# Kernel tuning notes

Measured on AMD Instinct MI355X. Metric: run time of the kernel, lower is better.

Reference implementation:

```python
import jax, jax.numpy as jnp
import numpy as np

T_TOTAL = 90  # t_total init arg (static decode length)


def _gru_cell(x, h, w_ih, w_hh, b_ih, b_hh):
    # PyTorch nn.GRUCell math
    gi = x @ w_ih.T + b_ih
    gh = h @ w_hh.T + b_hh
    i_r, i_z, i_n = jnp.split(gi, 3, axis=-1)
    h_r, h_z, h_n = jnp.split(gh, 3, axis=-1)
    r = jax.nn.sigmoid(i_r + h_r)
    z = jax.nn.sigmoid(i_z + h_z)
    n = jnp.tanh(i_n + r * h_n)
    return (1.0 - z) * n + z * h


def setup_inputs() -> dict:
    key = jax.random.key(0)
    T, B, NX, H, NZ = 90, 2048, 144, 128, 128
    M1, M2 = 300, 200
    ks = jax.random.split(key, 24)
    def p(k, shape):
        return jax.random.normal(k, shape, dtype=jnp.float32) * 0.05
    return {
        "x": jax.random.normal(ks[0], (T, B, NX), dtype=jnp.float32),
        # encoder GRUCell (nx -> H)
        "w_ih_e": p(ks[1], (3 * H, NX)), "w_hh_e": p(ks[2], (3 * H, H)),
        "b_ih_e": p(ks[3], (3 * H,)),   "b_hh_e": p(ks[4], (3 * H,)),
        # encoder MLP (tanh) H->300->200
        "W1e": p(ks[5], (M1, H)),  "b1e": p(ks[6], (M1,)),
        "W2e": p(ks[7], (M2, M1)), "b2e": p(ks[8], (M2,)),
        # latent heads 200->NZ
        "Wmu": p(ks[9], (NZ, M2)),  "bmu": p(ks[10], (NZ,)),
        "Wlv": p(ks[11], (NZ, M2)), "blv": p(ks[12], (NZ,)),
        # decoder GRUCell (nx+nz -> H)
        "w_ih_d": p(ks[13], (3 * H, NX + NZ)), "w_hh_d": p(ks[14], (3 * H, H)),
        "b_ih_d": p(ks[15], (3 * H,)),          "b_hh_d": p(ks[16], (3 * H,)),
        # decoder MLP (tanh) H->300->200 and output 200->nx
        "W1d": p(ks[17], (M1, H)),  "b1d": p(ks[18], (M1,)),
        "W2d": p(ks[19], (M2, M1)), "b2d": p(ks[20], (M2,)),
        "Wo": p(ks[21], (NX, M2)),  "bo": p(ks[22], (NX,)),
    }


def reference(x, w_ih_e, w_hh_e, b_ih_e, b_hh_e, W1e, b1e, W2e, b2e,
              Wmu, bmu, Wlv, blv, w_ih_d, w_hh_d, b_ih_d, b_hh_d,
              W1d, b1d, W2d, b2d, Wo, bo):
    B = x.shape[1]
    H = w_hh_e.shape[1]
    h0 = jnp.zeros((B, H), dtype=x.dtype)

    # ---- encode: GRU over time, take last hidden ----
    def enc_step(h, xt):
        return _gru_cell(xt, h, w_ih_e, w_hh_e, b_ih_e, b_hh_e), None
    h_x, _ = jax.lax.scan(enc_step, h0, x)  # (B, H)
    he = jnp.tanh(h_x @ W1e.T + b1e)
    he = jnp.tanh(he @ W2e.T + b2e)
    mu = he @ Wmu.T + bmu
    logvar = he @ Wlv.T + blv
    z = mu  # eval mode: z = mu (no reparameterization noise)

    def dec_step(carry, _):
        hd, xp = carry
        rnn_in = jnp.concatenate([xp, z], axis=1)  # (B, NX+NZ)
        hd = _gru_cell(rnn_in, hd, w_ih_d, w_hh_d, b_ih_d, b_hh_d)
        m = jnp.tanh(hd @ W1d.T + b1d)
        m = jnp.tanh(m @ W2d.T + b2d)
        xi = m @ Wo.T + bo
        return (hd, xi), xi

    _, x_rec = jax.lax.scan(dec_step, (h0, x[0]), None, length=T_TOTAL)
    return x_rec, mu, logvar
```

## Files before the change

kernel.cpp:

```cpp
#include <hip/hip_runtime.h>
#include <cstddef>

#define T_STEPS 90
#define BT      2048
#define NXV     144
#define HV      128
#define NZV     128
#define M1V     300
#define M2V     200
#define NB      16
#define NTH     512

typedef __attribute__((ext_vector_type(8))) _Float16 half8v;
typedef __attribute__((ext_vector_type(4))) float f32x4;

constexpr int MTa[12]   = {24,24,19,13, 8, 8,24,24,24,19,13, 9};
constexpr int MREAL[12] = {384,384,300,200,128,128,384,384,384,300,200,144};
constexpr int KREAL[12] = {144,128,128,300,200,200,144,128,128,128,300,200};
constexpr int RSW[12]   = {144,128,128,300,200,200,272,272,128,128,300,200};
constexpr int COW[12]   = {  0,  0,  0,  0,  0,  0,  0,144,  0,  0,  0,  0};
constexpr int P13[13]   = {0,120,240,335,465,521,577,697,817,937,1032,1162,1225};
constexpr int NFRAG = 1225;

__device__ __forceinline__ float fsig(float v)  { return 1.0f / (1.0f + __expf(-v)); }
__device__ __forceinline__ float ftanh(float v) { return 1.0f - 2.0f / (__expf(2.0f * v) + 1.0f); }

__global__ void __launch_bounds__(64)
prep_frags(const float* __restrict__ w_ih_e, const float* __restrict__ w_hh_e,
           const float* __restrict__ W1e,    const float* __restrict__ W2e,
           const float* __restrict__ Wmu,    const float* __restrict__ Wlv,
           const float* __restrict__ w_ih_d, const float* __restrict__ w_hh_d,
           const float* __restrict__ W1d,    const float* __restrict__ W2d,
           const float* __restrict__ Wo,
           const float* __restrict__ b_ih_e, const float* __restrict__ b_hh_e,
           const float* __restrict__ b1e,    const float* __restrict__ b2e,
           const float* __restrict__ bmu,    const float* __restrict__ blv,
           const float* __restrict__ b_ih_d, const float* __restrict__ b_hh_d,
           const float* __restrict__ b1d,    const float* __restrict__ b2d,
           const float* __restrict__ bo,
           _Float16* __restrict__ ws)
{
    int f = blockIdx.x;
    int g = 0;
    while (g < 11 && f >= P13[g + 1]) ++g;
    int fl = f - P13[g];
    int MT = MTa[g];
    int kt = fl / MT, mt = fl - kt * MT;

    const float* W; const float* bias;
    switch (g) {
        case 0:  W = w_ih_e; bias = b_ih_e; break;
        case 1:  W = w_hh_e; bias = b_hh_e; break;
        case 2:  W = W1e;    bias = b1e;    break;
        case 3:  W = W2e;    bias = b2e;    break;
        case 4:  W = Wmu;    bias = bmu;    break;
        case 5:  W = Wlv;    bias = blv;    break;
        case 6:  W = w_ih_d; bias = nullptr; break;
        case 7:  W = w_ih_d; bias = b_ih_d; break;
        case 8:  W = w_hh_d; bias = b_hh_d; break;
        case 9:  W = W1d;    bias = b1d;    break;
        case 10: W = W2d;    bias = b2d;    break;
        default: W = Wo;     bias = bo;     break;
    }
    int l = threadIdx.x;
    int m  = mt * 16 + (l & 15);
    int kb = kt * 32 + (l >> 4) * 8;
    _Float16* dst = ws + (size_t)f * 512 + (size_t)l * 8;
    #pragma unroll
    for (int j = 0; j < 8; ++j) {
        int k = kb + j;
        float val = 0.0f;
        if (m < MREAL[g]) {
            if (k < KREAL[g]) val = W[(size_t)m * RSW[g] + COW[g] + k];
            else if (k == KREAL[g] && bias) val = bias[m];
        }
        dst[j] = (_Float16)val;
    }
}

template<int RS>
__device__ __forceinline__ void gate_gemm_reg(const half8v (&gw)[15],
                                              const _Float16* __restrict__ Bt,
                                              int l, f32x4 (&acc)[3])
{
    const int bo_ = (l & 15) * RS + ((l >> 4) << 3);
    #pragma unroll
    for (int kt = 0; kt < 5; ++kt) {
        half8v bf = *(const half8v*)(Bt + bo_ + kt * 32);
        #pragma unroll
        for (int j = 0; j < 3; ++j)
            acc[j] = __builtin_amdgcn_mfma_f32_16x16x32_f16(gw[kt * 3 + j], bf, acc[j], 0, 0, 0);
    }
}

template<int MT, int KT, int NT, int RS>
__device__ __forceinline__ void mlp_stream(const half8v* __restrict__ A,
                                           const _Float16* __restrict__ Bt,
                                           int w, int l, f32x4 (&acc)[NT])
{
    half8v af[NT * KT];
    #pragma unroll
    for (int i = 0; i < NT; ++i) {
        int mt = w + 8 * i;
        if (mt < MT) {
            #pragma unroll
            for (int kt = 0; kt < KT; ++kt)
                af[i * KT + kt] = A[(size_t)(kt * MT + mt) * 64 + l];
        }
    }
    const int bo_ = (l & 15) * RS + ((l >> 4) << 3);
    #pragma unroll
    for (int kt = 0; kt < KT; ++kt) {
        half8v bf = *(const half8v*)(Bt + bo_ + kt * 32);
        #pragma unroll
        for (int i = 0; i < NT; ++i) {
            int mt = w + 8 * i;
            if (mt < MT)
                acc[i] = __builtin_amdgcn_mfma_f32_16x16x32_f16(af[i * KT + kt], bf, acc[i], 0, 0, 0);
        }
    }
}

template<int MT, int KT, int NT, int RS>
__device__ __forceinline__ void mlp_lds(const _Float16* __restrict__ Alds,
                                        const _Float16* __restrict__ Bt,
                                        int w, int l, f32x4 (&acc)[NT])
{
    const int bo_ = (l & 15) * RS + ((l >> 4) << 3);
    #pragma unroll
    for (int kt = 0; kt < KT; ++kt) {
        half8v bf = *(const half8v*)(Bt + bo_ + kt * 32);
        #pragma unroll
        for (int i = 0; i < NT; ++i) {
            int mt = w + 8 * i;
            if (mt < MT) {
                half8v af = *(const half8v*)(Alds + ((size_t)(kt * MT + mt) * 64 + l) * 8);
                acc[i] = __builtin_amdgcn_mfma_f32_16x16x32_f16(af, bf, acc[i], 0, 0, 0);
            }
        }
    }
}

template<int MT, int NT, int RS>
__device__ __forceinline__ void write_tanhN(const f32x4 (&acc)[NT], int Mreal,
                                            _Float16* __restrict__ T, int w, int l)
{
    int b = l & 15, q4 = (l >> 4) << 2;
    #pragma unroll
    for (int i = 0; i < NT; ++i) {
        int mt = w + 8 * i;
        if (mt < MT) {
            #pragma unroll
            for (int r = 0; r < 4; ++r) {
                int m = mt * 16 + q4 + r;
                if (m < Mreal) T[b * RS + m] = (_Float16)ftanh(acc[i][r]);
            }
        }
    }
}

__global__ void __launch_bounds__(NTH, 2)
vae_mfma(const float* __restrict__ x, const half8v* __restrict__ wsv,
         float* __restrict__ out)
{
    __shared__ __align__(16) _Float16 xT [NB * 168];
    __shared__ __align__(16) _Float16 hT [NB * 168];
    __shared__ __align__(16) _Float16 m1T[NB * 328];
    __shared__ __align__(16) _Float16 m2T[NB * 232];
    __shared__ __align__(16) _Float16 g10L[130 * 512];

    const int tid = threadIdx.x;
    const int w = tid >> 6, l = tid & 63;
    const int bbase = blockIdx.x * NB;
    const size_t XREC_SZ = (size_t)T_STEPS * BT * NXV;
    const size_t MU_OFF = XREC_SZ;
    const size_t LV_OFF = XREC_SZ + (size_t)BT * NZV;
    const f32x4 z4 = {0.f, 0.f, 0.f, 0.f};

#define AHI(g) (wsv + (size_t)P13[g] * 64)

    auto load_x = [&](int t, float xr[5]) {
        #pragma unroll
        for (int u = 0; u < 5; ++u) {
            int i = u * NTH + tid;
            if (i < NB * NXV)
                xr[u] = __builtin_nontemporal_load(
                    &x[(size_t)t * (BT * NXV) + (size_t)(bbase + i / NXV) * NXV + (i % NXV)]);
        }
    };
    auto store_x = [&](const float xr[5]) {
        #pragma unroll
        for (int u = 0; u < 5; ++u) {
            int i = u * NTH + tid;
            if (i < NB * NXV) {
                int b2 = i / NXV, k = i - b2 * NXV;
                xT[b2 * 168 + k] = (_Float16)xr[u];
            }
        }
    };

    half8v gih[15], ghh[15];
    auto load_gates = [&](const half8v* Gih, const half8v* Ghh) {
        #pragma unroll
        for (int kt = 0; kt < 5; ++kt) {
            #pragma unroll
            for (int j = 0; j < 3; ++j) {
                gih[kt * 3 + j] = Gih[(size_t)(kt * 24 + w + 8 * j) * 64 + l];
                ghh[kt * 3 + j] = Ghh[(size_t)(kt * 24 + w + 8 * j) * 64 + l];
            }
        }
    };

    float hreg[4] = {0.f, 0.f, 0.f, 0.f};
    auto gru_combine = [&](const f32x4 (&ai)[3], const f32x4 (&ah)[3]) {
        #pragma unroll
        for (int r = 0; r < 4; ++r) {
            float rr = fsig(ai[0][r] + ah[0][r]);
            float zz = fsig(ai[1][r] + ah[1][r]);
            float nn = ftanh(ai[2][r] + rr * ah[2][r]);
            hreg[r] = (1.f - zz) * nn + zz * hreg[r];
        }
    };
    auto write_h = [&]() {
        int jb = 16 * w + ((l >> 4) << 2), b = l & 15;
        #pragma unroll
        for (int r = 0; r < 4; ++r) hT[b * 168 + jb + r] = (_Float16)hreg[r];
    };

    for (int i = tid; i < NB * 168; i += NTH) { xT[i] = (_Float16)0.f; hT[i] = (_Float16)0.f; }
    for (int i = tid; i < NB * 328; i += NTH) m1T[i] = (_Float16)0.f;
    for (int i = tid; i < NB * 232; i += NTH) m2T[i] = (_Float16)0.f;
    for (int i = tid; i < 130 * 64; i += NTH)
        *(half8v*)(g10L + (size_t)i * 8) = AHI(10)[i];
    load_gates(AHI(0), AHI(1));
    float xr[5] = {0, 0, 0, 0, 0};
    load_x(0, xr);
    __syncthreads();
    if (tid < NB) {
        xT [tid * 168 + 144] = (_Float16)1.f;
        hT [tid * 168 + 128] = (_Float16)1.f;
        m1T[tid * 328 + 300] = (_Float16)1.f;
        m2T[tid * 232 + 200] = (_Float16)1.f;
    }
    store_x(xr);
    load_x(1, xr);
    __syncthreads();

    for (int t = 0; t < T_STEPS; ++t) {
        f32x4 ai[3] = {z4, z4, z4}, ah[3] = {z4, z4, z4};
        gate_gemm_reg<168>(gih, xT, l, ai);
        gate_gemm_reg<168>(ghh, hT, l, ah);
        gru_combine(ai, ah);
        __syncthreads();
        write_h();
        if (t + 1 < T_STEPS) {
            store_x(xr);
            if (t + 2 < T_STEPS) load_x(t + 2, xr);
        }
        __syncthreads();
    }

    {
        f32x4 a1[3] = {z4, z4, z4};
        mlp_stream<19, 5, 3, 168>(AHI(2), hT, w, l, a1);
        write_tanhN<19, 3, 328>(a1, M1V, m1T, w, l);
        __syncthreads();
        f32x4 a2[2] = {z4, z4};
        mlp_stream<13, 10, 2, 328>(AHI(3), m1T, w, l, a2);
        write_tanhN<13, 2, 232>(a2, M2V, m2T, w, l);
        __syncthreads();
        f32x4 am[1] = {z4}, av[1] = {z4};
        mlp_stream<8, 7, 1, 232>(AHI(4), m2T, w, l, am);
        mlp_stream<8, 7, 1, 232>(AHI(5), m2T, w, l, av);
        __syncthreads();
        int b = l & 15, q4 = (l >> 4) << 2;
        int m = w * 16 + q4;
        __builtin_nontemporal_store(am[0], (f32x4*)&out[MU_OFF + (size_t)(bbase + b) * NZV + m]);
        __builtin_nontemporal_store(av[0], (f32x4*)&out[LV_OFF + (size_t)(bbase + b) * NZV + m]);
        #pragma unroll
        for (int r = 0; r < 4; ++r)
            m1T[b * 328 + m + r] = (_Float16)am[0][r];
    }

    f32x4 gzr[3] = {z4, z4, z4};
    {
        for (int i = tid; i < NB * HV; i += NTH) {
            int b2 = i >> 7, j = i & 127;
            hT[b2 * 168 + j] = (_Float16)0.f;
        }
        if (tid < NB) m1T[tid * 328 + 128] = (_Float16)1.f;
        float xr0[5] = {0, 0, 0, 0, 0};
        load_x(0, xr0);
        store_x(xr0);
        __syncthreads();
        mlp_stream<24, 5, 3, 328>(AHI(7), m1T, w, l, gzr);
        load_gates(AHI(6), AHI(8));
        #pragma unroll
        for (int r = 0; r < 4; ++r) hreg[r] = 0.f;
    }
    __syncthreads();

    for (int t = 0; t < T_STEPS; ++t) {
        f32x4 ai[3], ah[3];
        #pragma unroll
        for (int i = 0; i < 3; ++i) { ai[i] = gzr[i]; ah[i] = z4; }
        gate_gemm_reg<168>(gih, xT, l, ai);
        gate_gemm_reg<168>(ghh, hT, l, ah);
        gru_combine(ai, ah);
        __syncthreads();
        write_h();
        __syncthreads();
        f32x4 a1[3] = {z4, z4, z4};
        mlp_stream<19, 5, 3, 168>(AHI(9), hT, w, l, a1);
        write_tanhN<19, 3, 328>(a1, M1V, m1T, w, l);
        __syncthreads();
        f32x4 a2[2] = {z4, z4};
        mlp_lds<13, 10, 2, 328>(g10L, m1T, w, l, a2);
        write_tanhN<13, 2, 232>(a2, M2V, m2T, w, l);
        __syncthreads();
        f32x4 ao[2] = {z4, z4};
        mlp_stream<9, 7, 2, 232>(AHI(11), m2T, w, l, ao);
        {
            int b = l & 15, q4 = (l >> 4) << 2;
            #pragma unroll
            for (int i2 = 0; i2 < 2; ++i2) {
                int mt = w + 8 * i2;
                if (mt < 9) {
                    int m = mt * 16 + q4;
                    __builtin_nontemporal_store(ao[i2],
                        (f32x4*)&out[(size_t)t * (BT * NXV) + (size_t)(bbase + b) * NXV + m]);
                    #pragma unroll
                    for (int r = 0; r < 4; ++r)
                        xT[b * 168 + m + r] = (_Float16)ao[i2][r];
                }
            }
        }
        __syncthreads();
    }
#undef AHI
}

extern "C" void kernel_launch(void* const* d_in, const int* in_sizes, int n_in,
                              void* d_out, int out_size, void* d_ws, size_t ws_size,
                              hipStream_t stream) {
    (void)in_sizes; (void)n_in; (void)out_size; (void)ws_size;
    const float* p[23];
    for (int i = 0; i < 23; ++i) p[i] = (const float*)d_in[i];
    _Float16* ws = (_Float16*)d_ws;

    prep_frags<<<dim3(NFRAG), dim3(64), 0, stream>>>(
        p[1], p[2], p[5], p[7], p[9], p[11], p[13], p[14], p[17], p[19], p[21],
        p[3], p[4], p[6], p[8], p[10], p[12], p[15], p[16], p[18], p[20], p[22],
        ws);

    vae_mfma<<<dim3(BT / NB), dim3(NTH), 0, stream>>>(
        p[0], (const half8v*)ws, (float*)d_out);
}
```

Before: 882.5 us.

## Double-buffer GRU hidden/input LDS tiles to drop a barrier per step

Adds ping-pong buffers for the hidden and input tiles in LDS, so each GRU step writes the new state into the other buffer and one __syncthreads per timestep can be removed in both encoder and decoder loops. It also vectorises the x loads (float4) and the fp16 LDS stores (half4), and shrinks the LDS-resident W2d fragment cache by one K-tile, streaming the last tile from global memory before the MFMA to cut LDS footprint. The cost is extra LDS for the second buffers and more care about buffer parity at the encoder/decoder handoff.

```diff
diff --git a/kernel.cpp b/kernel.cpp
--- a/kernel.cpp
+++ b/kernel.cpp
@@ -12,6 +12,7 @@
 #define NTH     512
 
 typedef __attribute__((ext_vector_type(8))) _Float16 half8v;
+typedef __attribute__((ext_vector_type(4))) _Float16 half4v;
 typedef __attribute__((ext_vector_type(4))) float f32x4;
 
 constexpr int MTa[12]   = {24,24,19,13, 8, 8,24,24,24,19,13, 9};
@@ -142,7 +143,7 @@
 }
 
 template<int MT, int NT, int RS>
-__device__ __forceinline__ void write_tanhN(const f32x4 (&acc)[NT], int Mreal,
+__device__ __forceinline__ void write_tanhV(const f32x4 (&acc)[NT], int Mreal,
                                             _Float16* __restrict__ T, int w, int l)
 {
     int b = l & 15, q4 = (l >> 4) << 2;
@@ -150,10 +151,12 @@
     for (int i = 0; i < NT; ++i) {
         int mt = w + 8 * i;
         if (mt < MT) {
-            #pragma unroll
-            for (int r = 0; r < 4; ++r) {
-                int m = mt * 16 + q4 + r;
-                if (m < Mreal) T[b * RS + m] = (_Float16)ftanh(acc[i][r]);
+            int m0 = mt * 16 + q4;
+            if (m0 < Mreal) {
+                half4v v;
+                #pragma unroll
+                for (int r = 0; r < 4; ++r) v[r] = (_Float16)ftanh(acc[i][r]);
+                *(half4v*)&T[b * RS + m0] = v;
             }
         }
     }
@@ -163,11 +166,11 @@
 vae_mfma(const float* __restrict__ x, const half8v* __restrict__ wsv,
          float* __restrict__ out)
 {
-    __shared__ __align__(16) _Float16 xT [NB * 168];
-    __shared__ __align__(16) _Float16 hT [NB * 168];
+    __shared__ __align__(16) _Float16 xT [2][NB * 168];
+    __shared__ __align__(16) _Float16 hT [2][NB * 168];
     __shared__ __align__(16) _Float16 m1T[NB * 328];
     __shared__ __align__(16) _Float16 m2T[NB * 232];
-    __shared__ __align__(16) _Float16 g10L[130 * 512];
+    __shared__ __align__(16) _Float16 g10L[117 * 512];
 
     const int tid = threadIdx.x;
     const int w = tid >> 6, l = tid & 63;
@@ -179,22 +182,27 @@
 
 #define AHI(g) (wsv + (size_t)P13[g] * 64)
 
-    auto load_x = [&](int t, float xr[5]) {
-        #pragma unroll
-        for (int u = 0; u < 5; ++u) {
-            int i = u * NTH + tid;
-            if (i < NB * NXV)
-                xr[u] = __builtin_nontemporal_load(
-                    &x[(size_t)t * (BT * NXV) + (size_t)(bbase + i / NXV) * NXV + (i % NXV)]);
-        }
-    };
-    auto store_x = [&](const float xr[5]) {
-        #pragma unroll
-        for (int u = 0; u < 5; ++u) {
-            int i = u * NTH + tid;
-            if (i < NB * NXV) {
-                int b2 = i / NXV, k = i - b2 * NXV;
-                xT[b2 * 168 + k] = (_Float16)xr[u];
+    auto load_x4 = [&](int t, f32x4 xr4[2]) {
+        #pragma unroll
+        for (int uu = 0; uu < 2; ++uu) {
+            int idx = uu * NTH + tid;
+            if (idx < NB * (NXV / 4)) {
+                int b2 = idx / (NXV / 4), k4 = idx - b2 * (NXV / 4);
+                xr4[uu] = __builtin_nontemporal_load(
+                    (const f32x4*)&x[(size_t)t * (BT * NXV) + (size_t)(bbase + b2) * NXV + 4 * k4]);
+            }
+        }
+    };
+    auto store_x4 = [&](_Float16* dst, const f32x4 xr4[2]) {
+        #pragma unroll
+        for (int uu = 0; uu < 2; ++uu) {
+            int idx = uu * NTH + tid;
+            if (idx < NB * (NXV / 4)) {
+                int b2 = idx / (NXV / 4), k4 = idx - b2 * (NXV / 4);
+                half4v v;
+                #pragma unroll
+                for (int r = 0; r < 4; ++r) v[r] = (_Float16)xr4[uu][r];
+                *(half4v*)&dst[b2 * 168 + 4 * k4] = v;
             }
         }
     };
@@ -221,53 +229,57 @@
             hreg[r] = (1.f - zz) * nn + zz * hreg[r];
         }
     };
-    auto write_h = [&]() {
+    auto write_h = [&](int p) {
         int jb = 16 * w + ((l >> 4) << 2), b = l & 15;
-        #pragma unroll
-        for (int r = 0; r < 4; ++r) hT[b * 168 + jb + r] = (_Float16)hreg[r];
-    };
-
-    for (int i = tid; i < NB * 168; i += NTH) { xT[i] = (_Float16)0.f; hT[i] = (_Float16)0.f; }
+        half4v v;
+        #pragma unroll
+        for (int r = 0; r < 4; ++r) v[r] = (_Float16)hreg[r];
+        *(half4v*)&hT[p][b * 168 + jb] = v;
+    };
+
+    for (int i = tid; i < 2 * NB * 168; i += NTH) { ((_Float16*)xT)[i] = (_Float16)0.f; ((_Float16*)hT)[i] = (_Float16)0.f; }
     for (int i = tid; i < NB * 328; i += NTH) m1T[i] = (_Float16)0.f;
     for (int i = tid; i < NB * 232; i += NTH) m2T[i] = (_Float16)0.f;
-    for (int i = tid; i < 130 * 64; i += NTH)
+    for (int i = tid; i < 117 * 64; i += NTH)
         *(half8v*)(g10L + (size_t)i * 8) = AHI(10)[i];
     load_gates(AHI(0), AHI(1));
-    float xr[5] = {0, 0, 0, 0, 0};
-    load_x(0, xr);
+    f32x4 xr4[2] = {z4, z4};
+    load_x4(0, xr4);
     __syncthreads();
     if (tid < NB) {
-        xT [tid * 168 + 144] = (_Float16)1.f;
-        hT [tid * 168 + 128] = (_Float16)1.f;
+        xT[0][tid * 168 + 144] = (_Float16)1.f;
+        xT[1][tid * 168 + 144] = (_Float16)1.f;
+        hT[0][tid * 168 + 128] = (_Float16)1.f;
+        hT[1][tid * 168 + 128] = (_Float16)1.f;
         m1T[tid * 328 + 300] = (_Float16)1.f;
         m2T[tid * 232 + 200] = (_Float16)1.f;
     }
-    store_x(xr);
-    load_x(1, xr);
+    store_x4(xT[0], xr4);
+    load_x4(1, xr4);
     __syncthreads();
 
     for (int t = 0; t < T_STEPS; ++t) {
+        int p = t & 1;
         f32x4 ai[3] = {z4, z4, z4}, ah[3] = {z4, z4, z4};
-        gate_gemm_reg<168>(gih, xT, l, ai);
-        gate_gemm_reg<168>(ghh, hT, l, ah);
+        gate_gemm_reg<168>(gih, xT[p], l, ai);
+        gate_gemm_reg<168>(ghh, hT[p], l, ah);
         gru_combine(ai, ah);
-        __syncthreads();
-        write_h();
+        write_h(p ^ 1);
         if (t + 1 < T_STEPS) {
-            store_x(xr);
-            if (t + 2 < T_STEPS) load_x(t + 2, xr);
+            store_x4(xT[p ^ 1], xr4);
+            if (t + 2 < T_STEPS) load_x4(t + 2, xr4);
         }
         __syncthreads();
     }
 
     {
         f32x4 a1[3] = {z4, z4, z4};
-        mlp_stream<19, 5, 3, 168>(AHI(2), hT, w, l, a1);
-        write_tanhN<19, 3, 328>(a1, M1V, m1T, w, l);
+        mlp_stream<19, 5, 3, 168>(AHI(2), hT[0], w, l, a1);
+        write_tanhV<19, 3, 328>(a1, M1V, m1T, w, l);
         __syncthreads();
         f32x4 a2[2] = {z4, z4};
         mlp_stream<13, 10, 2, 328>(AHI(3), m1T, w, l, a2);
-        write_tanhN<13, 2, 232>(a2, M2V, m2T, w, l);
+        write_tanhV<13, 2, 232>(a2, M2V, m2T, w, l);
         __syncthreads();
         f32x4 am[1] = {z4}, av[1] = {z4};
         mlp_stream<8, 7, 1, 232>(AHI(4), m2T, w, l, am);
@@ -277,21 +289,22 @@
         int m = w * 16 + q4;
         __builtin_nontemporal_store(am[0], (f32x4*)&out[MU_OFF + (size_t)(bbase + b) * NZV + m]);
         __builtin_nontemporal_store(av[0], (f32x4*)&out[LV_OFF + (size_t)(bbase + b) * NZV + m]);
-        #pragma unroll
-        for (int r = 0; r < 4; ++r)
-            m1T[b * 328 + m + r] = (_Float16)am[0][r];
+        half4v zv;
+        #pragma unroll
+        for (int r = 0; r < 4; ++r) zv[r] = (_Float16)am[0][r];
+        *(half4v*)&m1T[b * 328 + m] = zv;
     }
 
     f32x4 gzr[3] = {z4, z4, z4};
     {
         for (int i = tid; i < NB * HV; i += NTH) {
             int b2 = i >> 7, j = i & 127;
-            hT[b2 * 168 + j] = (_Float16)0.f;
+            hT[0][b2 * 168 + j] = (_Float16)0.f;
         }
         if (tid < NB) m1T[tid * 328 + 128] = (_Float16)1.f;
-        float xr0[5] = {0, 0, 0, 0, 0};
-        load_x(0, xr0);
-        store_x(xr0);
+        f32x4 xr0[2] = {z4, z4};
+        load_x4(0, xr0);
+        store_x4(xT[0], xr0);
         __syncthreads();
         mlp_stream<24, 5, 3, 328>(AHI(7), m1T, w, l, gzr);
         load_gates(AHI(6), AHI(8));
@@ -301,22 +314,35 @@
     __syncthreads();
 
     for (int t = 0; t < T_STEPS; ++t) {
+        int q = t & 1;
         f32x4 ai[3], ah[3];
         #pragma unroll
         for (int i = 0; i < 3; ++i) { ai[i] = gzr[i]; ah[i] = z4; }
-        gate_gemm_reg<168>(gih, xT, l, ai);
-        gate_gemm_reg<168>(ghh, hT, l, ah);
+        gate_gemm_reg<168>(gih, xT[0], l, ai);
+        gate_gemm_reg<168>(ghh, hT[q], l, ah);
         gru_combine(ai, ah);
-        __syncthreads();
-        write_h();
+        write_h(q ^ 1);
         __syncthreads();
         f32x4 a1[3] = {z4, z4, z4};
-        mlp_stream<19, 5, 3, 168>(AHI(9), hT, w, l, a1);
-        write_tanhN<19, 3, 328>(a1, M1V, m1T, w, l);
-        __syncthreads();
+        mlp_stream<19, 5, 3, 168>(AHI(9), hT[q ^ 1], w, l, a1);
+        write_tanhV<19, 3, 328>(a1, M1V, m1T, w, l);
+        __syncthreads();
+        half8v w2f9[2];
+        #pragma unroll
+        for (int i = 0; i < 2; ++i)
+            if (w + 8 * i < 13)
+                w2f9[i] = AHI(10)[(size_t)(9 * 13 + w + 8 * i) * 64 + l];
         f32x4 a2[2] = {z4, z4};
-        mlp_lds<13, 10, 2, 328>(g10L, m1T, w, l, a2);
-        write_tanhN<13, 2, 232>(a2, M2V, m2T, w, l);
+        mlp_lds<13, 9, 2, 328>(g10L, m1T, w, l, a2);
+        {
+            const int bo2 = (l & 15) * 328 + ((l >> 4) << 3);
+            half8v bf = *(const half8v*)(m1T + bo2 + 9 * 32);
+            #pragma unroll
+            for (int i = 0; i < 2; ++i)
+                if (w + 8 * i < 13)
+                    a2[i] = __builtin_amdgcn_mfma_f32_16x16x32_f16(w2f9[i], bf, a2[i], 0, 0, 0);
+        }
+        write_tanhV<13, 2, 232>(a2, M2V, m2T, w, l);
         __syncthreads();
         f32x4 ao[2] = {z4, z4};
         mlp_stream<9, 7, 2, 232>(AHI(11), m2T, w, l, ao);
@@ -329,9 +355,10 @@
                     int m = mt * 16 + q4;
                     __builtin_nontemporal_store(ao[i2],
                         (f32x4*)&out[(size_t)t * (BT * NXV) + (size_t)(bbase + b) * NXV + m]);
+                    half4v vh;
                     #pragma unroll
-                    for (int r = 0; r < 4; ++r)
-                        xT[b * 168 + m + r] = (_Float16)ao[i2][r];
+                    for (int r = 0; r < 4; ++r) vh[r] = (_Float16)ao[i2][r];
+                    *(half4v*)&xT[0][b * 168 + m] = vh;
                 }
             }
         }
```

Result: slower. 906.6 us (+2.7%).
